# Kernel optimization log

Measured on AMD Instinct MI355X. Metric: run time of the kernel, lower is better.

## Reference

```python
import jax, jax.numpy as jnp
import numpy as np

B, L, D, H = 2, 2048, 1024, 16
DH = D // H
SCALE = DH ** -0.5


def setup_inputs() -> dict:
    key = jax.random.key(0)
    k1, k2, k3 = jax.random.split(key, 3)
    x = jax.random.normal(k1, (B, L, D), dtype=jnp.float32)
    W_qkv = jax.random.normal(k2, (D, 3 * D), dtype=jnp.float32) * 0.02
    b_qkv = jnp.zeros((3 * D,), dtype=jnp.float32)
    W_proj = jax.random.normal(k3, (D, D), dtype=jnp.float32) * 0.02
    b_proj = jnp.zeros((D,), dtype=jnp.float32)
    return {"x": x, "W_qkv": W_qkv, "b_qkv": b_qkv, "W_proj": W_proj, "b_proj": b_proj}


def reference(x, W_qkv, b_qkv, W_proj, b_proj):
    b, l, d = x.shape
    # QKV projection: [B,L,3D] -> [3,B,H,L,DH] matching 'b n (three h d) -> three b h n d'
    qkv = (x @ W_qkv + b_qkv).reshape(b, l, 3, H, DH).transpose(2, 0, 3, 1, 4)
    q, k, v = qkv[0], qkv[1], qkv[2]
    # Causal scores. Chunking in the original is purely a scheduling detail;
    # masks are indexed by absolute row positions, so full attention is identical.
    scores = jnp.einsum('bhqd,bhkd->bhqk', q, k) * SCALE
    mask = jnp.triu(jnp.ones((l, l), dtype=bool), 1)  # True above diagonal
    neg_inf = jnp.finfo(scores.dtype).min
    scores = jnp.where(mask, neg_inf, scores)
    m = jnp.max(scores, axis=-1, keepdims=True)
    e = jnp.where(mask, 0.0, jnp.exp(scores - m))
    attn = e / (jnp.sum(e, axis=-1, keepdims=True) + 1e-6)
    out = jnp.einsum('bhqk,bhkd->bhqd', attn, v)  # [B,H,L,DH]
    out = out.transpose(0, 2, 1, 3).reshape(b, l, d)  # 'b h n d -> b n (h d)'
    return out @ W_proj + b_proj
```

## Files before the change

### kernel.cpp

```cpp
#include <hip/hip_runtime.h>


typedef __bf16 bf16x8 __attribute__((ext_vector_type(8)));
typedef float  f32x4  __attribute__((ext_vector_type(4)));
typedef unsigned short bhalf;
typedef unsigned int   uint32;

#define B_  2
#define L_  2048
#define D_  1024
#define H_  16
#define DH_ 64

#define GPTR(p) ((const __attribute__((address_space(1))) void*)(p))
#define SPTR(p) ((__attribute__((address_space(3))) void*)(p))

static __device__ __forceinline__ float bf2f(bhalf u) {
    union { uint32 u; float f; } x; x.u = ((uint32)u) << 16; return x.f;
}
static __device__ __forceinline__ bhalf f2bf(float f) {
    union { float f; uint32 u; } x; x.f = f;
    uint32 r = x.u + 0x7FFFu + ((x.u >> 16) & 1u);
    return (bhalf)(r >> 16);
}

__global__ void detect_dtype(const uint32* __restrict__ xw, int* __restrict__ flag) {
    int t = threadIdx.x;
    uint32 w = xw[t];
    uint32 e = (w >> 7) & 0xFFu;
    int g = (e < 0x6Fu || e > 0x84u) ? 1 : 0;
#pragma unroll
    for (int off = 32; off; off >>= 1) g += __shfl_xor(g, off);
    if (t == 0) *flag = (g > 16) ? 0 : 1;
}

__global__ void conv_bf16(const void* __restrict__ in, bhalf* __restrict__ out,
                          int n4, const int* __restrict__ flag) {
    const bool isb = (*flag != 0);
    for (int i = blockIdx.x * blockDim.x + threadIdx.x; i < n4;
         i += gridDim.x * blockDim.x) {
        if (isb) {
            ((uint2*)out)[i] = ((const uint2*)in)[i];
        } else {
            float4 v = ((const float4*)in)[i];
            uint2 o;
            o.x = (uint32)f2bf(v.x) | ((uint32)f2bf(v.y) << 16);
            o.y = (uint32)f2bf(v.z) | ((uint32)f2bf(v.w) << 16);
            ((uint2*)out)[i] = o;
        }
    }
}

__global__ void tr_conv(const void* __restrict__ in, bhalf* __restrict__ out,
                        int R, int C, const int* __restrict__ flag) {
    __shared__ bhalf t[32][33];
    const bool isb = (*flag != 0);
    int bx = blockIdx.x, by = blockIdx.y;
    int tx = threadIdx.x, ty = threadIdx.y;
#pragma unroll
    for (int i = 0; i < 32; i += 8) {
        size_t idx = (size_t)(by * 32 + ty + i) * C + bx * 32 + tx;
        t[ty + i][tx] = isb ? ((const bhalf*)in)[idx]
                            : f2bf(((const float*)in)[idx]);
    }
    __syncthreads();
#pragma unroll
    for (int i = 0; i < 32; i += 8)
        out[(size_t)(bx * 32 + ty + i) * R + by * 32 + tx] = t[tx][ty + i];
}

template <int MODE>
__global__ __launch_bounds__(256) void gemm_bt(
        const bhalf* __restrict__ A, const bhalf* __restrict__ Bt,
        const void* __restrict__ bias,
        void* __restrict__ C0, bhalf* __restrict__ Qb,
        bhalf* __restrict__ Kb, bhalf* __restrict__ Vtb,
        int M, int N, int K, const int* __restrict__ flag) {
    __shared__ bhalf As[128 * 32];
    __shared__ bhalf Bs[128 * 32];
    const bool isb = (*flag != 0);
    const int tid  = threadIdx.x;
    const int w    = tid >> 6, lane = tid & 63;
    const int g    = lane >> 4, cl = lane & 15;
    const int m0   = blockIdx.y * 128, n0 = blockIdx.x * 128;
    const int wr   = (w >> 1) * 64, wc = (w & 1) * 64;

    f32x4 acc[4][4] = {};

    const bhalf* a0 = A  + (size_t)m0 * K;
    const bhalf* b0 = Bt + (size_t)n0 * K;

    for (int kk = 0; kk < K; kk += 32) {
        __syncthreads();
#pragma unroll
        for (int r = 0; r < 2; r++) {
            int c = r * 256 + tid;
            int row = c >> 2, p = c & 3;
            int gch = p ^ (row & 3);
            __builtin_amdgcn_global_load_lds(
                GPTR(a0 + (size_t)row * K + kk + gch * 8),
                SPTR(As + (r * 256 + w * 64) * 8), 16, 0, 0);
            __builtin_amdgcn_global_load_lds(
                GPTR(b0 + (size_t)row * K + kk + gch * 8),
                SPTR(Bs + (r * 256 + w * 64) * 8), 16, 0, 0);
        }
        __syncthreads();

        bf16x8 af[4], bf[4];
#pragma unroll
        for (int i = 0; i < 4; i++) {
            int ra = wr + i * 16 + cl;
            af[i] = *(const bf16x8*)(As + ra * 32 + ((g ^ (ra & 3)) * 8));
            int rb = wc + i * 16 + cl;
            bf[i] = *(const bf16x8*)(Bs + rb * 32 + ((g ^ (rb & 3)) * 8));
        }
#pragma unroll
        for (int i = 0; i < 4; i++)
#pragma unroll
            for (int j = 0; j < 4; j++)
                acc[i][j] = __builtin_amdgcn_mfma_f32_16x16x32_bf16(
                    af[i], bf[j], acc[i][j], 0, 0, 0);
    }

#pragma unroll
    for (int i = 0; i < 4; i++) {
#pragma unroll
        for (int j = 0; j < 4; j++) {
            int nn = n0 + wc + j * 16 + cl;
            float bv = isb ? bf2f(((const bhalf*)bias)[nn])
                           : ((const float*)bias)[nn];
#pragma unroll
            for (int r = 0; r < 4; r++) {
                int mm = m0 + wr + i * 16 + g * 4 + r;
                float v = acc[i][j][r] + bv;
                if (MODE == 0) {
                    if (isb) ((bhalf*)C0)[(size_t)mm * N + nn] = f2bf(v);
                    else     ((float*)C0)[(size_t)mm * N + nn] = v;
                } else {
                    bhalf o = f2bf(v);
                    int b = mm >> 11, l = mm & 2047;
                    int three = nn >> 10, rem = nn & 1023;
                    int h = rem >> 6, dh = rem & 63;
                    size_t bh = (size_t)(b * 16 + h);
                    if (three == 0)      Qb [(bh * 2048 + l) * 64 + dh] = o;
                    else if (three == 1) Kb [(bh * 2048 + l) * 64 + dh] = o;
                    else                 Vtb[(bh * 64 + dh) * 2048 + l] = o;
                }
            }
        }
    }
}


#define STAGE(BUF, KT) do {                                                   \
    int ktv = (KT);                                                           \
    _Pragma("unroll")                                                         \
    for (int r = 0; r < 4; r++) {                                             \
        int c = r * 256 + tid;                                                \
        int row = c >> 3, p = c & 7;                                          \
        int fsw = (row & 3) | (((row >> 3) & 1) << 2);                        \
        __builtin_amdgcn_global_load_lds(                                     \
            GPTR(Kp + (size_t)(ktv * 128 + row) * 64 + (p ^ fsw) * 8),        \
            SPTR(Ks[BUF] + (r * 256 + w * 64) * 8), 16, 0, 0);                \
    }                                                                         \
    _Pragma("unroll")                                                         \
    for (int r = 0; r < 4; r++) {                                             \
        int c = r * 256 + tid;                                                \
        int row = c >> 4, p = c & 15;                                         \
        __builtin_amdgcn_global_load_lds(                                     \
            GPTR(Vt + (size_t)row * L_ + ktv * 128 + (p ^ (row & 15)) * 8),   \
            SPTR(Vs[BUF] + (r * 256 + w * 64) * 8), 16, 0, 0);                \
    }                                                                         \
} while (0)

#define ATTN_TILE(BUF, KT, QF, QLANE, MVAR, LVAR, OACC, MASK) do {            \
    f32x4 p8[8] = {};                                                         \
    _Pragma("unroll")                                                         \
    for (int s = 0; s < 2; s++) {                                             \
        bf16x8 kf[8];                                                         \
        _Pragma("unroll")                                                     \
        for (int j = 0; j < 8; j++) {                                         \
            int row = (j >> 1) * 32 + (cl >> 2) * 8 + (j & 1) * 4 + (cl & 3); \
            int fsw = (row & 3) | (((row >> 3) & 1) << 2);                    \
            int ch = s * 4 + g;                                               \
            kf[j] = *(const bf16x8*)(Ks[BUF] + row * 64 + ((ch ^ fsw) * 8));  \
        }                                                                     \
        __builtin_amdgcn_s_setprio(1);                                        \
        _Pragma("unroll")                                                     \
        for (int j = 0; j < 8; j++)                                           \
            p8[j] = __builtin_amdgcn_mfma_f32_16x16x32_bf16(                  \
                kf[j], QF[s], p8[j], 0, 0, 0);                                \
        __builtin_amdgcn_s_setprio(0);                                        \
    }                                                                         \
    float mx = -__builtin_inff();                                             \
    _Pragma("unroll")                                                         \
    for (int j = 0; j < 8; j++) {                                             \
        _Pragma("unroll")                                                     \
        for (int r = 0; r < 4; r++) {                                         \
            float v = p8[j][r] * 0.125f;                                      \
            if (MASK) {                                                       \
                int ka = (KT) * 128 + (j >> 1) * 32 + g * 8 + ((j & 1) << 2) + r; \
                v = (ka > (QLANE)) ? -__builtin_inff() : v;                   \
            }                                                                 \
            p8[j][r] = v;                                                     \
            mx = fmaxf(mx, v);                                                \
        }                                                                     \
    }                                                                         \
    mx = fmaxf(mx, __shfl_xor(mx, 16));                                       \
    mx = fmaxf(mx, __shfl_xor(mx, 32));                                       \
    float mnew = fmaxf(MVAR, mx);                                             \
    float alpha = __expf(MVAR - mnew);                                        \
    MVAR = mnew;                                                              \
    _Pragma("unroll")                                                         \
    for (int r = 0; r < 4; r++) {                                             \
        float ar = __shfl(alpha, g * 4 + r);                                  \
        _Pragma("unroll")                                                     \
        for (int dj = 0; dj < 4; dj++) OACC[dj][r] *= ar;                     \
    }                                                                         \
    float ls = 0.f;                                                           \
    _Pragma("unroll")                                                         \
    for (int j = 0; j < 8; j++)                                               \
        _Pragma("unroll")                                                     \
        for (int r = 0; r < 4; r++) {                                         \
            float e = __expf(p8[j][r] - mnew);                                \
            p8[j][r] = e;                                                     \
            ls += e;                                                          \
        }                                                                     \
    ls += __shfl_xor(ls, 16);                                                 \
    ls += __shfl_xor(ls, 32);                                                 \
    LVAR = LVAR * alpha + ls;                                                 \
    _Pragma("unroll")                                                         \
    for (int ks = 0; ks < 4; ks++) {                                          \
        bf16x8 pf;                                                            \
        _Pragma("unroll")                                                     \
        for (int e = 0; e < 8; e++)                                           \
            pf[e] = (__bf16)p8[2 * ks + (e >> 2)][e & 3];                     \
        bf16x8 vf[4];                                                         \
        _Pragma("unroll")                                                     \
        for (int dj = 0; dj < 4; dj++) {                                      \
            int vrow = dj * 16 + cl;                                          \
            int ch = ks * 4 + g;                                              \
            vf[dj] = *(const bf16x8*)(Vs[BUF] + vrow * 128 + ((ch ^ (vrow & 15)) * 8)); \
        }                                                                     \
        __builtin_amdgcn_s_setprio(1);                                        \
        _Pragma("unroll")                                                     \
        for (int dj = 0; dj < 4; dj++)                                        \
            OACC[dj] = __builtin_amdgcn_mfma_f32_16x16x32_bf16(               \
                pf, vf[dj], OACC[dj], 0, 0, 0);                               \
        __builtin_amdgcn_s_setprio(0);                                        \
    }                                                                         \
} while (0)

__global__ __launch_bounds__(256, 2) void attn_fwd(
        const bhalf* __restrict__ Qb, const bhalf* __restrict__ Kb,
        const bhalf* __restrict__ Vtb, bhalf* __restrict__ Ob) {
    __shared__ bhalf Ks[2][128 * 64];
    __shared__ bhalf Vs[2][64 * 128];

    const int bid  = blockIdx.x;
    const int xcd  = bid & 7, slot = bid >> 3;
    const int bx   = slot & 15;
    const int bh   = xcd + 8 * (slot >> 4);
    const int qbA  = 31 - bx;
    const int qbB  = bx;

    const int tid = threadIdx.x;
    const int w = tid >> 6, lane = tid & 63;
    const int g = lane >> 4, cl = lane & 15;

    const bhalf* Q  = Qb  + (size_t)bh * L_ * DH_;
    const bhalf* Kp = Kb  + (size_t)bh * L_ * DH_;
    const bhalf* Vt = Vtb + (size_t)bh * DH_ * L_;

    const int q0A = qbA * 64 + w * 16, qlA = q0A + cl;
    const int q0B = qbB * 64 + w * 16, qlB = q0B + cl;

    bf16x8 qfA[2], qfB[2];
#pragma unroll
    for (int s = 0; s < 2; s++) {
        qfA[s] = *(const bf16x8*)(Q + (size_t)(q0A + cl) * 64 + s * 32 + g * 8);
        qfB[s] = *(const bf16x8*)(Q + (size_t)(q0B + cl) * 64 + s * 32 + g * 8);
    }

    f32x4 oA[4] = {}, oB[4] = {};
    float mA = -__builtin_inff(), lA = 0.f;
    float mB = -__builtin_inff(), lB = 0.f;

    const int nktA = (qbA >> 1) + 1;
    const int nktB = (qbB >> 1) + 1;
    const int ntot = nktA + nktB;

    STAGE(0, 0);
    __syncthreads();

    for (int t = 0; t < ntot; ++t) {
        int cur = t & 1;
        if (t + 1 < ntot) {
            int tn = t + 1;
            int ktn = (tn < nktA) ? tn : (tn - nktA);
            STAGE(cur ^ 1, ktn);
        }
        if (t < nktA) {
            ATTN_TILE(cur, t, qfA, qlA, mA, lA, oA, (t == nktA - 1));
        } else {
            int kt = t - nktA;
            ATTN_TILE(cur, kt, qfB, qlB, mB, lB, oB, (kt == nktB - 1));
        }
        __syncthreads();
    }

    const int b = bh >> 4, h = bh & 15;
#pragma unroll
    for (int r = 0; r < 4; r++) {
        float lrA = __shfl(lA, g * 4 + r);
        float lrB = __shfl(lB, g * 4 + r);
        float invA = 1.f / (lrA + 1e-6f);
        float invB = 1.f / (lrB + 1e-6f);
        int qrA = q0A + g * 4 + r, qrB = q0B + g * 4 + r;
#pragma unroll
        for (int dj = 0; dj < 4; dj++) {
            Ob[((size_t)b * L_ + qrA) * D_ + h * 64 + dj * 16 + cl] =
                f2bf(oA[dj][r] * invA);
            Ob[((size_t)b * L_ + qrB) * D_ + h * 64 + dj * 16 + cl] =
                f2bf(oB[dj][r] * invB);
        }
    }
}

extern "C" void kernel_launch(void* const* d_in, const int* in_sizes, int n_in,
                              void* d_out, int out_size, void* d_ws, size_t ws_size,
                              hipStream_t stream) {
    const void* x     = d_in[0];
    const void* Wqkv  = d_in[1];
    const void* bqkv  = d_in[2];
    const void* Wproj = d_in[3];
    const void* bproj = d_in[4];

    char* ws = (char*)d_ws;
    const size_t SZ_FLG = 256;
    const size_t SZ_WQT = (size_t)3 * D_ * D_ * 2;
    const size_t SZ_WPT = (size_t)D_ * D_ * 2;
    const size_t SZ_X   = (size_t)B_ * L_ * D_ * 2;
    const size_t SZ_BUF = (size_t)B_ * H_ * L_ * DH_ * 2;

    int*   flag = (int*)ws;
    bhalf* Wq_t = (bhalf*)(ws + SZ_FLG);
    bhalf* Wp_t = (bhalf*)(ws + SZ_FLG + SZ_WQT);
    bhalf* Xb   = (bhalf*)(ws + SZ_FLG + SZ_WQT + SZ_WPT);
    bhalf* Qbuf = (bhalf*)(ws + SZ_FLG + SZ_WQT + SZ_WPT + SZ_X);
    bhalf* Kbuf = (bhalf*)(ws + SZ_FLG + SZ_WQT + SZ_WPT + SZ_X + SZ_BUF);
    bhalf* Vtbf = (bhalf*)(ws + SZ_FLG + SZ_WQT + SZ_WPT + SZ_X + 2 * SZ_BUF);
    bhalf* Obuf = (bhalf*)(ws + SZ_FLG + SZ_WQT + SZ_WPT + SZ_X + 3 * SZ_BUF);

    const int M = B_ * L_;

    detect_dtype<<<1, 64, 0, stream>>>((const uint32*)x, flag);

    conv_bf16<<<2048, 256, 0, stream>>>(x, Xb, (B_ * L_ * D_) / 4, flag);
    tr_conv<<<dim3(3 * D_ / 32, D_ / 32), dim3(32, 8), 0, stream>>>(
        Wqkv, Wq_t, D_, 3 * D_, flag);
    tr_conv<<<dim3(D_ / 32, D_ / 32), dim3(32, 8), 0, stream>>>(
        Wproj, Wp_t, D_, D_, flag);

    gemm_bt<1><<<dim3(3 * D_ / 128, M / 128), 256, 0, stream>>>(
        Xb, Wq_t, bqkv, nullptr, Qbuf, Kbuf, Vtbf, M, 3 * D_, D_, flag);

    attn_fwd<<<dim3(512), 256, 0, stream>>>(Qbuf, Kbuf, Vtbf, Obuf);

    gemm_bt<0><<<dim3(D_ / 128, M / 128), 256, 0, stream>>>(
        Obuf, Wp_t, bproj, d_out, nullptr, nullptr, nullptr, M, D_, D_, flag);
}
```

Measured before the change: 140.6 us.

## Double-buffer GEMM LDS tiles and prefetch next K-slice during MFMA

Converts the bf16 GEMM main loop to double-buffered LDS. The next K-slice is issued via global_load_lds before the current slice's MFMAs run, which removes one barrier per iteration and hides global load latency. It also changes the LDS swizzle to a rotate-style pattern (p - row - row>>2) to reduce bank conflicts, and raises wave priority around the MFMA block. The cost is twice the LDS use, which may lower occupancy, and there is no wait on the async loads other than the trailing syncthreads.

```diff
diff --git a/kernel.cpp b/kernel.cpp
--- a/kernel.cpp
+++ b/kernel.cpp
@@ -69,6 +69,23 @@
         out[(size_t)(bx * 32 + ty + i) * R + by * 32 + tx] = t[tx][ty + i];
 }
 
+
+#define GSTAGE(BUF, KK) do {                                                  \
+    int kko = (KK);                                                           \
+    _Pragma("unroll")                                                         \
+    for (int r = 0; r < 2; r++) {                                             \
+        int c = r * 256 + tid;                                                \
+        int row = c >> 2, p = c & 3;                                          \
+        int gch = (p - row - (row >> 2)) & 3;                                 \
+        __builtin_amdgcn_global_load_lds(                                     \
+            GPTR(a0 + (size_t)row * K + kko + gch * 8),                       \
+            SPTR(As[BUF] + (r * 256 + w * 64) * 8), 16, 0, 0);                \
+        __builtin_amdgcn_global_load_lds(                                     \
+            GPTR(b0 + (size_t)row * K + kko + gch * 8),                       \
+            SPTR(Bs[BUF] + (r * 256 + w * 64) * 8), 16, 0, 0);                \
+    }                                                                         \
+} while (0)
+
 template <int MODE>
 __global__ __launch_bounds__(256) void gemm_bt(
         const bhalf* __restrict__ A, const bhalf* __restrict__ Bt,
@@ -76,8 +93,8 @@
         void* __restrict__ C0, bhalf* __restrict__ Qb,
         bhalf* __restrict__ Kb, bhalf* __restrict__ Vtb,
         int M, int N, int K, const int* __restrict__ flag) {
-    __shared__ bhalf As[128 * 32];
-    __shared__ bhalf Bs[128 * 32];
+    __shared__ bhalf As[2][128 * 32];
+    __shared__ bhalf Bs[2][128 * 32];
     const bool isb = (*flag != 0);
     const int tid  = threadIdx.x;
     const int w    = tid >> 6, lane = tid & 63;
@@ -90,36 +107,34 @@
     const bhalf* a0 = A  + (size_t)m0 * K;
     const bhalf* b0 = Bt + (size_t)n0 * K;
 
-    for (int kk = 0; kk < K; kk += 32) {
-        __syncthreads();
-#pragma unroll
-        for (int r = 0; r < 2; r++) {
-            int c = r * 256 + tid;
-            int row = c >> 2, p = c & 3;
-            int gch = p ^ (row & 3);
-            __builtin_amdgcn_global_load_lds(
-                GPTR(a0 + (size_t)row * K + kk + gch * 8),
-                SPTR(As + (r * 256 + w * 64) * 8), 16, 0, 0);
-            __builtin_amdgcn_global_load_lds(
-                GPTR(b0 + (size_t)row * K + kk + gch * 8),
-                SPTR(Bs + (r * 256 + w * 64) * 8), 16, 0, 0);
-        }
-        __syncthreads();
-
-        bf16x8 af[4], bf[4];
+    GSTAGE(0, 0);
+    __syncthreads();
+
+    const int nk = K >> 5;
+    for (int t = 0; t < nk; ++t) {
+        int cur = t & 1;
+        if (t + 1 < nk) GSTAGE(cur ^ 1, (t + 1) << 5);
+
+        bf16x8 af[4], bf4[4];
 #pragma unroll
         for (int i = 0; i < 4; i++) {
             int ra = wr + i * 16 + cl;
-            af[i] = *(const bf16x8*)(As + ra * 32 + ((g ^ (ra & 3)) * 8));
+            af[i]  = *(const bf16x8*)(As[cur] + ra * 32 +
+                                      (((g + ra + (ra >> 2)) & 3) * 8));
             int rb = wc + i * 16 + cl;
-            bf[i] = *(const bf16x8*)(Bs + rb * 32 + ((g ^ (rb & 3)) * 8));
-        }
+            bf4[i] = *(const bf16x8*)(Bs[cur] + rb * 32 +
+                                      (((g + rb + (rb >> 2)) & 3) * 8));
+        }
+        __builtin_amdgcn_s_setprio(1);
 #pragma unroll
         for (int i = 0; i < 4; i++)
 #pragma unroll
             for (int j = 0; j < 4; j++)
                 acc[i][j] = __builtin_amdgcn_mfma_f32_16x16x32_bf16(
-                    af[i], bf[j], acc[i][j], 0, 0, 0);
+                    af[i], bf4[j], acc[i][j], 0, 0, 0);
+        __builtin_amdgcn_s_setprio(0);
+
+        __syncthreads();
     }
 
 #pragma unroll
```

Measured after the change: 134.1 us. 4.6% less time.
